# Kernel tuning notes

Measured on AMD Instinct MI355X. Metric: run time of the kernel, lower is better.

## Reference

```python
import jax, jax.numpy as jnp
import numpy as np

H = 132  # hidden size hard-coded in SpatialRelationLayer

def _mlp(x, w1, b1, w2, b2, w3, b3):
    # FCBlock: 2 hidden layers of width 132 with ReLU, then linear out;
    # NNNet wraps it with sigmoid(out * 5)
    h = jax.nn.relu(x @ w1 + b1)
    h = jax.nn.relu(h @ w2 + b2)
    return jax.nn.sigmoid((h @ w3 + b3) * 5.0)

def _mlp_params(key, din, dout):
    k1, k2, k3 = jax.random.split(key, 3)
    def lin(k, i, o):
        kw, kb = jax.random.split(k)
        s = 1.0 / np.sqrt(i)
        return (jax.random.uniform(kw, (i, o), jnp.float32, -s, s),
                jax.random.uniform(kb, (o,), jnp.float32, -s, s))
    w1, b1 = lin(k1, din, H)
    w2, b2 = lin(k2, H, H)
    w3, b3 = lin(k3, H, dout)
    return w1, b1, w2, b2, w3, b3

def setup_inputs() -> dict:
    key = jax.random.key(0)
    b, N, D0, D1, D2 = 8, 128, 128, 128, 64
    O0, O1, O2 = 64, 64, 64
    kP, kQ, kR, kp, kq, kr = jax.random.split(key, 6)
    inp = {
        "P": jax.random.normal(kP, (b, D0), jnp.float32),
        "Q": jax.random.normal(kQ, (b, N, D1), jnp.float32),
        "R": jax.random.normal(kR, (b, N, N, D2), jnp.float32),
    }
    for name, k, din, dout in (("p", kp, D0 + D1, O0),
                               ("q", kq, D1 + D0 + 2 * D2, O1),
                               ("r", kr, D2 + 2 * D1, O2)):
        w1, b1, w2, b2, w3, b3 = _mlp_params(k, din, dout)
        inp.update({f"{name}_w1": w1, f"{name}_b1": b1,
                    f"{name}_w2": w2, f"{name}_b2": b2,
                    f"{name}_w3": w3, f"{name}_b3": b3})
    return inp

def reference(P, Q, R,
              p_w1, p_b1, p_w2, p_b2, p_w3, p_b3,
              q_w1, q_b1, q_w2, q_b2, q_w3, q_b3,
              r_w1, r_b1, r_w2, r_b2, r_w3, r_b3):
    b, N, D1 = Q.shape
    # P branch: global max over objects, concat with P
    P_inputs = jnp.concatenate([jnp.max(Q, axis=1), P], axis=1)  # [b, D1+D0]
    P_out = _mlp(P_inputs, p_w1, p_b1, p_w2, p_b2, p_w3, p_b3)
    # Q branch: broadcast P per-object, max-reduce relations over each axis
    P_exp = jnp.broadcast_to(P[:, None, :], (b, N, P.shape[1]))  # [b,N,D0]
    R_red0 = jnp.max(R, axis=1)  # [b,N,D2]
    R_red1 = jnp.max(R, axis=2)  # [b,N,D2]
    Q_inputs = jnp.concatenate([P_exp, Q, R_red0, R_red1], axis=2)
    Q_out = _mlp(Q_inputs, q_w1, q_b1, q_w2, q_b2, q_w3, q_b3)
    # R branch: pairwise broadcast of Q along both axes, concat with R
    Q0 = jnp.broadcast_to(Q[:, None, :, :], (b, N, N, D1))  # repeat along dim 1
    Q1 = jnp.broadcast_to(Q[:, :, None, :], (b, N, N, D1))  # repeat along dim 2
    R_inputs = jnp.concatenate([R, Q0, Q1], axis=-1)  # [b,N,N,D2+2*D1]
    R_out = _mlp(R_inputs, r_w1, r_b1, r_w2, r_b2, r_w3, r_b3)
    return (P_out, Q_out, R_out)
```

## Files before the change

kernel.cpp:

```cpp
#include <hip/hip_runtime.h>

typedef _Float16 f16;
typedef f16 f16x8 __attribute__((ext_vector_type(8)));
typedef f16 f16x4 __attribute__((ext_vector_type(4)));
typedef float f32x4 __attribute__((ext_vector_type(4)));

#define MFMA16(a, b, c) __builtin_amdgcn_mfma_f32_16x16x32_f16(a, b, c, 0, 0, 0)

#define OFF_RW1A 0
#define OFF_RW2  10240
#define OFF_RW3  35840
#define OFF_QW1  46080
#define OFF_QW2  87040
#define OFF_QW3  112640
#define OFF_PW1  122880
#define OFF_PW2  163840
#define OFF_PW3  189440
#define PACK_BYTES 399360

#define PREP_BLOCKS 2419

struct InPtrs { const float* p[21]; };

__device__ const int g_mSrc[9] = {15, 17, 19, 9, 11, 13, 3, 5, 7};
__device__ const int g_mK0[9]  = {0, 0, 0, 128, 0, 0, 0, 0, 0};
__device__ const int g_mK[9]   = {64, 132, 132, 256, 132, 132, 256, 132, 132};
__device__ const int g_mN[9]   = {132, 132, 64, 132, 132, 64, 132, 132, 64};
__device__ const int g_mNT[9]  = {10, 10, 4, 10, 10, 4, 10, 10, 4};
__device__ const int g_mDst[9] = {OFF_RW1A, OFF_RW2, OFF_RW3, OFF_QW1, OFF_QW2, OFF_QW3,
                                  OFF_PW1, OFF_PW2, OFF_PW3};
__device__ const int g_mBlk0[9] = {1024, 1029, 1042, 1047, 1067, 1080, 1085, 1105, 1118};

__global__ __launch_bounds__(256) void prep_kernel(InPtrs in, f16* __restrict__ wpk,
    float* __restrict__ c1, float* __restrict__ d1, float* __restrict__ e1q,
    float* __restrict__ qmax, float* __restrict__ red0, float* __restrict__ red1)
{
  __shared__ float sbuf[1024];
  const int mb = blockIdx.x, t = threadIdx.x;

  if (mb < 1024) {
    const int b = mb >> 7, j = mb & 127;
    const float* base = in.p[2] + (size_t)b * 128 * 8192 + (size_t)j * 64 + (t & 15) * 4;
    const int g = t >> 4;
    f32x4 mm[8];
    #pragma unroll
    for (int v = 0; v < 8; ++v)
      mm[v] = *(const f32x4*)(base + (size_t)(g + 16 * v) * 8192);
    #pragma unroll
    for (int s = 4; s > 0; s >>= 1)
      #pragma unroll
      for (int v = 0; v < 4; ++v)
        if (v < s) {
          mm[v][0] = fmaxf(mm[v][0], mm[v + s][0]);
          mm[v][1] = fmaxf(mm[v][1], mm[v + s][1]);
          mm[v][2] = fmaxf(mm[v][2], mm[v + s][2]);
          mm[v][3] = fmaxf(mm[v][3], mm[v + s][3]);
        }
    float* sr = sbuf + g * 64 + (t & 15) * 4;
    sr[0] = mm[0][0]; sr[1] = mm[0][1]; sr[2] = mm[0][2]; sr[3] = mm[0][3];
    __syncthreads();
    if (t < 64) {
      float m = sbuf[t];
      #pragma unroll
      for (int g2 = 1; g2 < 16; ++g2) m = fmaxf(m, sbuf[g2 * 64 + t]);
      red0[(size_t)mb * 64 + t] = m;
    }
  } else if (mb < 1123) {
    int mi = 8;
    while (mi > 0 && mb < g_mBlk0[mi]) --mi;
    const int NT = g_mNT[mi], K = g_mK[mi], N = g_mN[mi], K0 = g_mK0[mi];
    const int L = (mb - g_mBlk0[mi]) * 256 + t;
    const int lanes = ((K + 31) >> 5) * NT * 64;
    if (L < lanes) {
      const int lane = L & 63, tile = L >> 6;
      const int kk = tile / NT, nn = tile % NT;
      const float* src = in.p[g_mSrc[mi]];
      const int n = nn * 16 + (lane & 15);
      const int kb = kk * 32 + ((lane >> 4) << 3);
      f16x8 v;
      #pragma unroll
      for (int u = 0; u < 8; ++u) {
        const int k = kb + u;
        float f = (k < K && n < N) ? src[(size_t)(K0 + k) * N + n] : 0.f;
        v[u] = (f16)f;
      }
      *(f16x8*)(wpk + g_mDst[mi] + (size_t)L * 8) = v;
    }
  } else if (mb < 1131) {
    const int b = mb - 1123;
    const float* Qb = in.p[1] + (size_t)b * 128 * 128;
    const int d = t & 127, g = t >> 7;
    float m0 = -3.4e38f, m1 = m0, m2 = m0, m3 = m0;
    #pragma unroll
    for (int v = 0; v < 16; ++v) {
      const int i = g * 64 + v * 4;
      m0 = fmaxf(m0, Qb[(size_t)(i + 0) * 128 + d]);
      m1 = fmaxf(m1, Qb[(size_t)(i + 1) * 128 + d]);
      m2 = fmaxf(m2, Qb[(size_t)(i + 2) * 128 + d]);
      m3 = fmaxf(m3, Qb[(size_t)(i + 3) * 128 + d]);
    }
    sbuf[g * 128 + d] = fmaxf(fmaxf(m0, m1), fmaxf(m2, m3));
    __syncthreads();
    if (t < 128) qmax[b * 128 + t] = fmaxf(sbuf[t], sbuf[128 + t]);
  } else if (mb < 1139) {
    const int b = mb - 1131;
    const float* P = in.p[0]; const float* qw1 = in.p[9]; const float* qb1 = in.p[10];
    if (t < 160) {
      float a = 0.f;
      if (t < 132) {
        float a0 = 0.f, a1 = 0.f, a2 = 0.f, a3 = 0.f;
        for (int k = 0; k < 128; k += 4) {
          a0 += P[b * 128 + k + 0] * qw1[(size_t)(k + 0) * 132 + t];
          a1 += P[b * 128 + k + 1] * qw1[(size_t)(k + 1) * 132 + t];
          a2 += P[b * 128 + k + 2] * qw1[(size_t)(k + 2) * 132 + t];
          a3 += P[b * 128 + k + 3] * qw1[(size_t)(k + 3) * 132 + t];
        }
        a = qb1[t] + (a0 + a1) + (a2 + a3);
      }
      e1q[b * 160 + t] = a;
    }
  } else if (mb < 1395) {
    const int blk = mb - 1139;
    const float* Q = in.p[1]; const float* rw1 = in.p[15]; const float* rb1 = in.p[16];
    for (int o = t; o < 512; o += 256) sbuf[o] = Q[(size_t)blk * 512 + o];
    __syncthreads();
    if (t < 160) {
      float cc[4], dd[4];
      #pragma unroll
      for (int r = 0; r < 4; ++r) { cc[r] = 0.f; dd[r] = 0.f; }
      if (t < 132) {
        const float bb = rb1[t];
        #pragma unroll
        for (int r = 0; r < 4; ++r) cc[r] = bb;
        for (int k = 0; k < 128; ++k) {
          const float wc = rw1[(size_t)(192 + k) * 132 + t];
          const float wd = rw1[(size_t)(64 + k) * 132 + t];
          #pragma unroll
          for (int r = 0; r < 4; ++r) {
            cc[r] += sbuf[r * 128 + k] * wc;
            dd[r] += sbuf[r * 128 + k] * wd;
          }
        }
      }
      for (int r = 0; r < 4; ++r) {
        c1[(size_t)(blk * 4 + r) * 160 + t] = cc[r];
        d1[(size_t)(blk * 4 + r) * 160 + t] = dd[r];
      }
    }
  } else {
    const int blk = mb - 1395;
    const float* base = in.p[2] + (size_t)blk * 8192 + (t & 15) * 4;
    const int g = t >> 4;
    f32x4 mm[8];
    #pragma unroll
    for (int v = 0; v < 8; ++v)
      mm[v] = *(const f32x4*)(base + (size_t)(g + 16 * v) * 64);
    #pragma unroll
    for (int s = 4; s > 0; s >>= 1)
      #pragma unroll
      for (int v = 0; v < 4; ++v)
        if (v < s) {
          mm[v][0] = fmaxf(mm[v][0], mm[v + s][0]);
          mm[v][1] = fmaxf(mm[v][1], mm[v + s][1]);
          mm[v][2] = fmaxf(mm[v][2], mm[v + s][2]);
          mm[v][3] = fmaxf(mm[v][3], mm[v + s][3]);
        }
    float* sr = sbuf + g * 64 + (t & 15) * 4;
    sr[0] = mm[0][0]; sr[1] = mm[0][1]; sr[2] = mm[0][2]; sr[3] = mm[0][3];
    __syncthreads();
    if (t < 64) {
      float m = sbuf[t];
      #pragma unroll
      for (int g2 = 1; g2 < 16; ++g2) m = fmaxf(m, sbuf[g2 * 64 + t]);
      red1[(size_t)blk * 64 + t] = m;
    }
  }
}

__global__ __launch_bounds__(256, 2) void mainR_kernel(const float* __restrict__ R,
    const float* __restrict__ c1, const float* __restrict__ d1,
    const float* __restrict__ rb2, const float* __restrict__ rb3,
    const f16* __restrict__ wpk, float* __restrict__ outR)
{
  __shared__ f16 Xr[128][72];
  __shared__ f16 Hs[128][168];
  const int blk = blockIdx.x;
  const int t = threadIdx.x, lane = t & 63, w = t >> 6;
  const int wm = w >> 1, wn = w & 1;
  const int rbase = wm * 64, nbase = wn * 80;
  const int lr = (lane >> 4) << 2;
  const int lc = lane & 15;
  const int lk = (lane >> 4) << 3;

  const float* Rb = R + (size_t)blk * 8192;
  #pragma unroll
  for (int v = 0; v < 8; ++v) {
    const int quad = v * 256 + t;
    const int j = quad >> 4, kq = quad & 15;
    f32x4 rv = *(const f32x4*)(Rb + (size_t)j * 64 + kq * 4);
    f16x4 hv;
    hv[0] = (f16)rv[0]; hv[1] = (f16)rv[1]; hv[2] = (f16)rv[2]; hv[3] = (f16)rv[3];
    *(f16x4*)(&Xr[j][kq * 4]) = hv;
  }

  const int b = blk >> 7;
  const float* c1r = c1 + (size_t)blk * 160;
  const float* d1b = d1 + (size_t)b * 128 * 160;
  f32x4 acc[4][5];
  #pragma unroll
  for (int mi2 = 0; mi2 < 4; ++mi2) {
    #pragma unroll
    for (int n5 = 0; n5 < 5; ++n5) {
      const int n = nbase + n5 * 16 + lc;
      const float cv = c1r[n];
      #pragma unroll
      for (int r = 0; r < 4; ++r) {
        const int j = rbase + mi2 * 16 + lr + r;
        acc[mi2][n5][r] = cv + d1b[(size_t)j * 160 + n];
      }
    }
  }
  __syncthreads();
  const f16x8* W1p = (const f16x8*)(wpk + OFF_RW1A);
  #pragma unroll
  for (int kk = 0; kk < 2; ++kk) {
    f16x8 a[4];
    #pragma unroll
    for (int mi2 = 0; mi2 < 4; ++mi2)
      a[mi2] = *(const f16x8*)(&Xr[rbase + mi2 * 16 + lc][kk * 32 + lk]);
    #pragma unroll
    for (int n5 = 0; n5 < 5; ++n5) {
      const f16x8 bf = W1p[(size_t)(kk * 10 + wn * 5 + n5) * 64 + lane];
      #pragma unroll
      for (int mi2 = 0; mi2 < 4; ++mi2)
        acc[mi2][n5] = MFMA16(a[mi2], bf, acc[mi2][n5]);
    }
  }
  #pragma unroll
  for (int mi2 = 0; mi2 < 4; ++mi2)
    #pragma unroll
    for (int n5 = 0; n5 < 5; ++n5)
      #pragma unroll
      for (int r = 0; r < 4; ++r)
        Hs[rbase + mi2 * 16 + lr + r][nbase + n5 * 16 + lc] =
            (f16)fmaxf(acc[mi2][n5][r], 0.f);
  __syncthreads();

  #pragma unroll
  for (int mi2 = 0; mi2 < 4; ++mi2)
    #pragma unroll
    for (int n5 = 0; n5 < 5; ++n5) {
      const int n = nbase + n5 * 16 + lc;
      const float bv = (n < 132) ? rb2[n] : 0.f;
      #pragma unroll
      for (int r = 0; r < 4; ++r) acc[mi2][n5][r] = bv;
    }
  const f16x8* W2p = (const f16x8*)(wpk + OFF_RW2);
  #pragma unroll
  for (int kk = 0; kk < 5; ++kk) {
    f16x8 a[4];
    #pragma unroll
    for (int mi2 = 0; mi2 < 4; ++mi2)
      a[mi2] = *(const f16x8*)(&Hs[rbase + mi2 * 16 + lc][kk * 32 + lk]);
    #pragma unroll
    for (int n5 = 0; n5 < 5; ++n5) {
      const f16x8 bf = W2p[(size_t)(kk * 10 + wn * 5 + n5) * 64 + lane];
      #pragma unroll
      for (int mi2 = 0; mi2 < 4; ++mi2)
        acc[mi2][n5] = MFMA16(a[mi2], bf, acc[mi2][n5]);
    }
  }
  __syncthreads();
  #pragma unroll
  for (int mi2 = 0; mi2 < 4; ++mi2)
    #pragma unroll
    for (int n5 = 0; n5 < 5; ++n5)
      #pragma unroll
      for (int r = 0; r < 4; ++r)
        Hs[rbase + mi2 * 16 + lr + r][nbase + n5 * 16 + lc] =
            (f16)fmaxf(acc[mi2][n5][r], 0.f);
  __syncthreads();

  f32x4 acc3[4][2];
  const int n3base = wn * 32;
  #pragma unroll
  for (int mi2 = 0; mi2 < 4; ++mi2)
    #pragma unroll
    for (int n2 = 0; n2 < 2; ++n2) {
      const float bv = rb3[n3base + n2 * 16 + lc];
      #pragma unroll
      for (int r = 0; r < 4; ++r) acc3[mi2][n2][r] = bv;
    }
  const f16x8* W3p = (const f16x8*)(wpk + OFF_RW3);
  #pragma unroll
  for (int kk = 0; kk < 5; ++kk) {
    f16x8 a[4];
    #pragma unroll
    for (int mi2 = 0; mi2 < 4; ++mi2)
      a[mi2] = *(const f16x8*)(&Hs[rbase + mi2 * 16 + lc][kk * 32 + lk]);
    #pragma unroll
    for (int n2 = 0; n2 < 2; ++n2) {
      const f16x8 bf = W3p[(size_t)(kk * 4 + wn * 2 + n2) * 64 + lane];
      #pragma unroll
      for (int mi2 = 0; mi2 < 4; ++mi2)
        acc3[mi2][n2] = MFMA16(a[mi2], bf, acc3[mi2][n2]);
    }
  }
  float* Ro = outR + (size_t)blk * 8192;
  #pragma unroll
  for (int mi2 = 0; mi2 < 4; ++mi2)
    #pragma unroll
    for (int n2 = 0; n2 < 2; ++n2)
      #pragma unroll
      for (int r = 0; r < 4; ++r) {
        const int j = rbase + mi2 * 16 + lr + r;
        const int n = n3base + n2 * 16 + lc;
        Ro[(size_t)j * 64 + n] = 1.f / (1.f + __expf(-5.f * acc3[mi2][n2][r]));
      }
}

__global__ __launch_bounds__(256) void small_kernel(const float* __restrict__ P,
    const float* __restrict__ Q,
    const float* __restrict__ qb2, const float* __restrict__ qb3,
    const float* __restrict__ pb1, const float* __restrict__ pb2, const float* __restrict__ pb3,
    const f16* __restrict__ wpk, const float* __restrict__ e1q, const float* __restrict__ qmax,
    const float* __restrict__ red0, const float* __restrict__ red1,
    float* __restrict__ outP, float* __restrict__ outQ)
{
  __shared__ f16 Xc[64][72];
  __shared__ f16 Hs2[64][168];
  __shared__ f16 Wb[40960];
  const int blk = blockIdx.x;
  const bool isP = (blk == 16);
  const int t = threadIdx.x, lane = t & 63, w = t >> 6;
  const int wm = w >> 1, wn = w & 1;
  const int rb = wm * 32;
  const int lr = (lane >> 4) << 2, lc = lane & 15, lk = (lane >> 4) << 3;
  const int b = blk >> 1, x0 = (blk & 1) * 64;
  const f16* W1g = wpk + (isP ? OFF_PW1 : OFF_QW1);
  const f16* W2g = wpk + (isP ? OFF_PW2 : OFF_QW2);
  const f16* W3g = wpk + (isP ? OFF_PW3 : OFF_QW3);

  for (int f = w; f < 80; f += 4)
    *(f16x8*)(&Wb[f * 512 + lane * 8]) = *(const f16x8*)(W1g + (size_t)f * 512 + lane * 8);

  f32x4 acc[2][5];
  #pragma unroll
  for (int mi2 = 0; mi2 < 2; ++mi2)
    #pragma unroll
    for (int n5 = 0; n5 < 5; ++n5) {
      const int n = (wn * 5 + n5) * 16 + lc;
      const float cv = isP ? ((n < 132) ? pb1[n] : 0.f) : e1q[b * 160 + n];
      #pragma unroll
      for (int r = 0; r < 4; ++r) acc[mi2][n5][r] = cv;
    }

  for (int c = 0; c < 4; ++c) {
    __syncthreads();
    for (int o = t; o < 1024; o += 256) {
      const int rr = o >> 4, kq = o & 15;
      f32x4 v = {0.f, 0.f, 0.f, 0.f};
      if (isP) {
        if (rr < 8) {
          const float* s = (c < 2) ? (qmax + rr * 128 + c * 64) : (P + rr * 128 + (c - 2) * 64);
          v = *(const f32x4*)(s + kq * 4);
        }
      } else {
        const size_t rowg = (size_t)(b * 128 + x0 + rr);
        const float* s = (c < 2) ? (Q + rowg * 128 + c * 64)
                                 : (((c == 2) ? red0 : red1) + rowg * 64);
        v = *(const f32x4*)(s + kq * 4);
      }
      f16x4 hv;
      hv[0] = (f16)v[0]; hv[1] = (f16)v[1]; hv[2] = (f16)v[2]; hv[3] = (f16)v[3];
      *(f16x4*)(&Xc[rr][kq * 4]) = hv;
    }
    __syncthreads();
    #pragma unroll
    for (int kk = 0; kk < 2; ++kk) {
      f16x8 a[2];
      #pragma unroll
      for (int mi2 = 0; mi2 < 2; ++mi2)
        a[mi2] = *(const f16x8*)(&Xc[rb + mi2 * 16 + lc][kk * 32 + lk]);
      const int kg = c * 2 + kk;
      #pragma unroll
      for (int n5 = 0; n5 < 5; ++n5) {
        const f16x8 bf = *(const f16x8*)(&Wb[(kg * 10 + wn * 5 + n5) * 512 + lane * 8]);
        #pragma unroll
        for (int mi2 = 0; mi2 < 2; ++mi2)
          acc[mi2][n5] = MFMA16(a[mi2], bf, acc[mi2][n5]);
      }
    }
  }
  #pragma unroll
  for (int mi2 = 0; mi2 < 2; ++mi2)
    #pragma unroll
    for (int n5 = 0; n5 < 5; ++n5)
      #pragma unroll
      for (int r = 0; r < 4; ++r)
        Hs2[rb + mi2 * 16 + lr + r][(wn * 5 + n5) * 16 + lc] = (f16)fmaxf(acc[mi2][n5][r], 0.f);
  __syncthreads();

  for (int f = w; f < 50; f += 4)
    *(f16x8*)(&Wb[f * 512 + lane * 8]) = *(const f16x8*)(W2g + (size_t)f * 512 + lane * 8);
  for (int f = w; f < 20; f += 4)
    *(f16x8*)(&Wb[(50 + f) * 512 + lane * 8]) = *(const f16x8*)(W3g + (size_t)f * 512 + lane * 8);

  #pragma unroll
  for (int mi2 = 0; mi2 < 2; ++mi2)
    #pragma unroll
    for (int n5 = 0; n5 < 5; ++n5) {
      const int n = (wn * 5 + n5) * 16 + lc;
      const float bv = (n < 132) ? (isP ? pb2[n] : qb2[n]) : 0.f;
      #pragma unroll
      for (int r = 0; r < 4; ++r) acc[mi2][n5][r] = bv;
    }
  __syncthreads();
  #pragma unroll
  for (int kk = 0; kk < 5; ++kk) {
    f16x8 a[2];
    #pragma unroll
    for (int mi2 = 0; mi2 < 2; ++mi2)
      a[mi2] = *(const f16x8*)(&Hs2[rb + mi2 * 16 + lc][kk * 32 + lk]);
    #pragma unroll
    for (int n5 = 0; n5 < 5; ++n5) {
      const f16x8 bf = *(const f16x8*)(&Wb[(kk * 10 + wn * 5 + n5) * 512 + lane * 8]);
      #pragma unroll
      for (int mi2 = 0; mi2 < 2; ++mi2)
        acc[mi2][n5] = MFMA16(a[mi2], bf, acc[mi2][n5]);
    }
  }
  __syncthreads();
  #pragma unroll
  for (int mi2 = 0; mi2 < 2; ++mi2)
    #pragma unroll
    for (int n5 = 0; n5 < 5; ++n5)
      #pragma unroll
      for (int r = 0; r < 4; ++r)
        Hs2[rb + mi2 * 16 + lr + r][(wn * 5 + n5) * 16 + lc] = (f16)fmaxf(acc[mi2][n5][r], 0.f);
  __syncthreads();

  f32x4 acc3[2][2];
  #pragma unroll
  for (int mi2 = 0; mi2 < 2; ++mi2)
    #pragma unroll
    for (int j2 = 0; j2 < 2; ++j2) {
      const int n = (wn * 2 + j2) * 16 + lc;
      const float bv = isP ? pb3[n] : qb3[n];
      #pragma unroll
      for (int r = 0; r < 4; ++r) acc3[mi2][j2][r] = bv;
    }
  #pragma unroll
  for (int kk = 0; kk < 5; ++kk) {
    f16x8 a[2];
    #pragma unroll
    for (int mi2 = 0; mi2 < 2; ++mi2)
      a[mi2] = *(const f16x8*)(&Hs2[rb + mi2 * 16 + lc][kk * 32 + lk]);
    #pragma unroll
    for (int j2 = 0; j2 < 2; ++j2) {
      const f16x8 bf = *(const f16x8*)(&Wb[(50 + kk * 4 + wn * 2 + j2) * 512 + lane * 8]);
      #pragma unroll
      for (int mi2 = 0; mi2 < 2; ++mi2)
        acc3[mi2][j2] = MFMA16(a[mi2], bf, acc3[mi2][j2]);
    }
  }
  #pragma unroll
  for (int mi2 = 0; mi2 < 2; ++mi2)
    #pragma unroll
    for (int j2 = 0; j2 < 2; ++j2)
      #pragma unroll
      for (int r = 0; r < 4; ++r) {
        const int rr = rb + mi2 * 16 + lr + r;
        const int n = (wn * 2 + j2) * 16 + lc;
        const float s = 1.f / (1.f + __expf(-5.f * acc3[mi2][j2][r]));
        if (isP) {
          if (rr < 8) outP[rr * 64 + n] = s;
        } else {
          outQ[((size_t)(b * 128 + x0 + rr)) * 64 + n] = s;
        }
      }
}

extern "C" void kernel_launch(void* const* d_in, const int* in_sizes, int n_in,
                              void* d_out, int out_size, void* d_ws, size_t ws_size,
                              hipStream_t stream) {
  (void)in_sizes; (void)n_in; (void)out_size; (void)ws_size;
  InPtrs ip;
  for (int i = 0; i < 21; ++i) ip.p[i] = (const float*)d_in[i];

  char* ws = (char*)d_ws;
  f16* wpk = (f16*)ws;
  float* wsf = (float*)(ws + PACK_BYTES);
  float* c1 = wsf;
  float* d1 = wsf + 163840;
  float* e1q = wsf + 327680;
  float* qmax = wsf + 328960;
  float* red0 = wsf + 329984;
  float* red1 = wsf + 395520;

  float* outP = (float*)d_out;
  float* outQ = outP + 512;
  float* outR = outP + 66048;

  prep_kernel<<<dim3(PREP_BLOCKS), dim3(256), 0, stream>>>(ip, wpk, c1, d1, e1q, qmax, red0, red1);
  mainR_kernel<<<dim3(1024), dim3(256), 0, stream>>>((const float*)d_in[2], c1, d1,
      (const float*)d_in[18], (const float*)d_in[20], wpk, outR);
  small_kernel<<<dim3(17), dim3(256), 0, stream>>>((const float*)d_in[0], (const float*)d_in[1],
      (const float*)d_in[12], (const float*)d_in[14],
      (const float*)d_in[4], (const float*)d_in[6], (const float*)d_in[8],
      wpk, e1q, qmax, red0, red1, outP, outQ);
}
```

Before: 73.63 us.

## Merge R and Q/P MLP kernels into one launch with transposed MFMA operands

Combines the R-branch kernel and the small Q/P-branch kernel into a single launch of 1041 blocks that branch on block index and share one 80KB LDS pool. This removes a kernel launch and the tail gap between the two kernels. The MFMA operands are also swapped so each lane holds four consecutive output columns, which allows vectorized f32x4 bias and d1 loads, f16x4 LDS stores and f32x4 global output stores. The small-branch W1 staging is cut to half-size chunks to fit the shared pool. The larger static LDS allocation may lower occupancy for the R blocks.

```diff
diff --git a/kernel.cpp b/kernel.cpp
--- a/kernel.cpp
+++ b/kernel.cpp
@@ -177,308 +177,322 @@
   }
 }
 
-__global__ __launch_bounds__(256, 2) void mainR_kernel(const float* __restrict__ R,
-    const float* __restrict__ c1, const float* __restrict__ d1,
+__device__ __forceinline__ float sig5(float x) {
+  return 1.f / (1.f + __expf(-5.f * x));
+}
+
+__global__ __launch_bounds__(256, 2) void fused_kernel(
+    const float* __restrict__ R, const float* __restrict__ c1, const float* __restrict__ d1,
     const float* __restrict__ rb2, const float* __restrict__ rb3,
-    const f16* __restrict__ wpk, float* __restrict__ outR)
+    const f16* __restrict__ wpk, float* __restrict__ outR,
+    const float* __restrict__ P, const float* __restrict__ Q,
+    const float* __restrict__ qb2, const float* __restrict__ qb3,
+    const float* __restrict__ pb1, const float* __restrict__ pb2, const float* __restrict__ pb3,
+    const float* __restrict__ e1q, const float* __restrict__ qmax,
+    const float* __restrict__ red0, const float* __restrict__ red1,
+    float* __restrict__ outP, float* __restrict__ outQ)
 {
-  __shared__ f16 Xr[128][72];
-  __shared__ f16 Hs[128][168];
+  __shared__ __align__(16) char pool[81920];
   const int blk = blockIdx.x;
   const int t = threadIdx.x, lane = t & 63, w = t >> 6;
   const int wm = w >> 1, wn = w & 1;
-  const int rbase = wm * 64, nbase = wn * 80;
   const int lr = (lane >> 4) << 2;
   const int lc = lane & 15;
   const int lk = (lane >> 4) << 3;
 
-  const float* Rb = R + (size_t)blk * 8192;
-  #pragma unroll
-  for (int v = 0; v < 8; ++v) {
-    const int quad = v * 256 + t;
-    const int j = quad >> 4, kq = quad & 15;
-    f32x4 rv = *(const f32x4*)(Rb + (size_t)j * 64 + kq * 4);
-    f16x4 hv;
-    hv[0] = (f16)rv[0]; hv[1] = (f16)rv[1]; hv[2] = (f16)rv[2]; hv[3] = (f16)rv[3];
-    *(f16x4*)(&Xr[j][kq * 4]) = hv;
+  if (blk < 1024) {
+    f16 (*Xr)[72]  = (f16(*)[72])pool;
+    f16 (*Hs)[168] = (f16(*)[168])(pool + 18432);
+    const int rbase = wm * 64, nbase = wn * 80;
+
+    const float* Rb = R + (size_t)blk * 8192;
+    #pragma unroll
+    for (int v = 0; v < 8; ++v) {
+      const int quad = v * 256 + t;
+      const int j = quad >> 4, kq = quad & 15;
+      f32x4 rv = *(const f32x4*)(Rb + (size_t)j * 64 + kq * 4);
+      f16x4 hv;
+      hv[0] = (f16)rv[0]; hv[1] = (f16)rv[1]; hv[2] = (f16)rv[2]; hv[3] = (f16)rv[3];
+      *(f16x4*)(&Xr[j][kq * 4]) = hv;
+    }
+
+    const int b = blk >> 7;
+    const float* c1r = c1 + (size_t)blk * 160;
+    const float* d1b = d1 + (size_t)b * 128 * 160;
+    f32x4 acc[4][5];
+    f32x4 cvv[5];
+    #pragma unroll
+    for (int n5 = 0; n5 < 5; ++n5)
+      cvv[n5] = *(const f32x4*)(c1r + nbase + n5 * 16 + lr);
+    #pragma unroll
+    for (int mi2 = 0; mi2 < 4; ++mi2) {
+      const int j = rbase + mi2 * 16 + lc;
+      #pragma unroll
+      for (int n5 = 0; n5 < 5; ++n5) {
+        f32x4 dv = *(const f32x4*)(d1b + (size_t)j * 160 + nbase + n5 * 16 + lr);
+        acc[mi2][n5] = cvv[n5] + dv;
+      }
+    }
+    __syncthreads();
+    const f16x8* W1p = (const f16x8*)(wpk + OFF_RW1A);
+    #pragma unroll
+    for (int kk = 0; kk < 2; ++kk) {
+      f16x8 a[4];
+      #pragma unroll
+      for (int mi2 = 0; mi2 < 4; ++mi2)
+        a[mi2] = *(const f16x8*)(&Xr[rbase + mi2 * 16 + lc][kk * 32 + lk]);
+      #pragma unroll
+      for (int n5 = 0; n5 < 5; ++n5) {
+        const f16x8 bf = W1p[(size_t)(kk * 10 + wn * 5 + n5) * 64 + lane];
+        #pragma unroll
+        for (int mi2 = 0; mi2 < 4; ++mi2)
+          acc[mi2][n5] = MFMA16(bf, a[mi2], acc[mi2][n5]);
+      }
+    }
+    #pragma unroll
+    for (int mi2 = 0; mi2 < 4; ++mi2) {
+      const int j = rbase + mi2 * 16 + lc;
+      #pragma unroll
+      for (int n5 = 0; n5 < 5; ++n5) {
+        f16x4 hv;
+        #pragma unroll
+        for (int r = 0; r < 4; ++r) hv[r] = (f16)fmaxf(acc[mi2][n5][r], 0.f);
+        *(f16x4*)(&Hs[j][nbase + n5 * 16 + lr]) = hv;
+      }
+    }
+    __syncthreads();
+
+    #pragma unroll
+    for (int n5 = 0; n5 < 5; ++n5) {
+      const int nb = nbase + n5 * 16 + lr;
+      f32x4 bv = {0.f, 0.f, 0.f, 0.f};
+      if (nb < 132) bv = *(const f32x4*)(rb2 + nb);
+      #pragma unroll
+      for (int mi2 = 0; mi2 < 4; ++mi2) acc[mi2][n5] = bv;
+    }
+    const f16x8* W2p = (const f16x8*)(wpk + OFF_RW2);
+    #pragma unroll
+    for (int kk = 0; kk < 5; ++kk) {
+      f16x8 a[4];
+      #pragma unroll
+      for (int mi2 = 0; mi2 < 4; ++mi2)
+        a[mi2] = *(const f16x8*)(&Hs[rbase + mi2 * 16 + lc][kk * 32 + lk]);
+      #pragma unroll
+      for (int n5 = 0; n5 < 5; ++n5) {
+        const f16x8 bf = W2p[(size_t)(kk * 10 + wn * 5 + n5) * 64 + lane];
+        #pragma unroll
+        for (int mi2 = 0; mi2 < 4; ++mi2)
+          acc[mi2][n5] = MFMA16(bf, a[mi2], acc[mi2][n5]);
+      }
+    }
+    __syncthreads();
+    #pragma unroll
+    for (int mi2 = 0; mi2 < 4; ++mi2) {
+      const int j = rbase + mi2 * 16 + lc;
+      #pragma unroll
+      for (int n5 = 0; n5 < 5; ++n5) {
+        f16x4 hv;
+        #pragma unroll
+        for (int r = 0; r < 4; ++r) hv[r] = (f16)fmaxf(acc[mi2][n5][r], 0.f);
+        *(f16x4*)(&Hs[j][nbase + n5 * 16 + lr]) = hv;
+      }
+    }
+    __syncthreads();
+
+    f32x4 acc3[4][2];
+    const int n3base = wn * 32;
+    #pragma unroll
+    for (int n2 = 0; n2 < 2; ++n2) {
+      f32x4 bv = *(const f32x4*)(rb3 + n3base + n2 * 16 + lr);
+      #pragma unroll
+      for (int mi2 = 0; mi2 < 4; ++mi2) acc3[mi2][n2] = bv;
+    }
+    const f16x8* W3p = (const f16x8*)(wpk + OFF_RW3);
+    #pragma unroll
+    for (int kk = 0; kk < 5; ++kk) {
+      f16x8 a[4];
+      #pragma unroll
+      for (int mi2 = 0; mi2 < 4; ++mi2)
+        a[mi2] = *(const f16x8*)(&Hs[rbase + mi2 * 16 + lc][kk * 32 + lk]);
+      #pragma unroll
+      for (int n2 = 0; n2 < 2; ++n2) {
+        const f16x8 bf = W3p[(size_t)(kk * 4 + wn * 2 + n2) * 64 + lane];
+        #pragma unroll
+        for (int mi2 = 0; mi2 < 4; ++mi2)
+          acc3[mi2][n2] = MFMA16(bf, a[mi2], acc3[mi2][n2]);
+      }
+    }
+    float* Ro = outR + (size_t)blk * 8192;
+    #pragma unroll
+    for (int mi2 = 0; mi2 < 4; ++mi2) {
+      const int j = rbase + mi2 * 16 + lc;
+      #pragma unroll
+      for (int n2 = 0; n2 < 2; ++n2) {
+        f32x4 ov;
+        #pragma unroll
+        for (int r = 0; r < 4; ++r) ov[r] = sig5(acc3[mi2][n2][r]);
+        *(f32x4*)(Ro + (size_t)j * 64 + n3base + n2 * 16 + lr) = ov;
+      }
+    }
+  } else {
+    f16 (*Xc)[72]  = (f16(*)[72])pool;
+    f16 (*Hs2)[168] = (f16(*)[168])(pool + 9216);
+    f16* Wb = (f16*)(pool + 30720);
+    const int bs = blk - 1024;
+    const bool isP = (bs == 16);
+    const int rb = wm * 32;
+    const int b = bs >> 1, x0 = (bs & 1) * 64;
+    const f16* W1g = wpk + (isP ? OFF_PW1 : OFF_QW1);
+    const f16* W2g = wpk + (isP ? OFF_PW2 : OFF_QW2);
+    const f16* W3g = wpk + (isP ? OFF_PW3 : OFF_QW3);
+
+    f32x4 acc[2][5];
+    #pragma unroll
+    for (int n5 = 0; n5 < 5; ++n5) {
+      const int nb = wn * 80 + n5 * 16 + lr;
+      f32x4 cv = {0.f, 0.f, 0.f, 0.f};
+      if (isP) { if (nb < 132) cv = *(const f32x4*)(pb1 + nb); }
+      else cv = *(const f32x4*)(e1q + b * 160 + nb);
+      acc[0][n5] = cv; acc[1][n5] = cv;
+    }
+
+    for (int c = 0; c < 4; ++c) {
+      if ((c & 1) == 0) {
+        const int half = c >> 1;
+        for (int idx = t; idx < 40 * 64; idx += 256) {
+          const int f = idx >> 6, ln = idx & 63;
+          *(f16x8*)(&Wb[f * 512 + ln * 8]) =
+              *(const f16x8*)(W1g + (size_t)(half * 40 + f) * 512 + ln * 8);
+        }
+      }
+      for (int o = t; o < 1024; o += 256) {
+        const int rr = o >> 4, kq = o & 15;
+        f32x4 v = {0.f, 0.f, 0.f, 0.f};
+        if (isP) {
+          if (rr < 8) {
+            const float* s = (c < 2) ? (qmax + rr * 128 + c * 64) : (P + rr * 128 + (c - 2) * 64);
+            v = *(const f32x4*)(s + kq * 4);
+          }
+        } else {
+          const size_t rowg = (size_t)(b * 128 + x0 + rr);
+          const float* s = (c < 2) ? (Q + rowg * 128 + c * 64)
+                                   : (((c == 2) ? red0 : red1) + rowg * 64);
+          v = *(const f32x4*)(s + kq * 4);
+        }
+        f16x4 hv;
+        hv[0] = (f16)v[0]; hv[1] = (f16)v[1]; hv[2] = (f16)v[2]; hv[3] = (f16)v[3];
+        *(f16x4*)(&Xc[rr][kq * 4]) = hv;
+      }
+      __syncthreads();
+      #pragma unroll
+      for (int kk = 0; kk < 2; ++kk) {
+        f16x8 a[2];
+        #pragma unroll
+        for (int mi2 = 0; mi2 < 2; ++mi2)
+          a[mi2] = *(const f16x8*)(&Xc[rb + mi2 * 16 + lc][kk * 32 + lk]);
+        #pragma unroll
+        for (int n5 = 0; n5 < 5; ++n5) {
+          const int rel = ((c & 1) * 2 + kk) * 10 + wn * 5 + n5;
+          const f16x8 bf = *(const f16x8*)(&Wb[rel * 512 + lane * 8]);
+          #pragma unroll
+          for (int mi2 = 0; mi2 < 2; ++mi2)
+            acc[mi2][n5] = MFMA16(bf, a[mi2], acc[mi2][n5]);
+        }
+      }
+      __syncthreads();
+    }
+    #pragma unroll
+    for (int mi2 = 0; mi2 < 2; ++mi2) {
+      const int j = rb + mi2 * 16 + lc;
+      #pragma unroll
+      for (int n5 = 0; n5 < 5; ++n5) {
+        f16x4 hv;
+        #pragma unroll
+        for (int r = 0; r < 4; ++r) hv[r] = (f16)fmaxf(acc[mi2][n5][r], 0.f);
+        *(f16x4*)(&Hs2[j][wn * 80 + n5 * 16 + lr]) = hv;
+      }
+    }
+    for (int idx = t; idx < 50 * 64; idx += 256) {
+      const int f = idx >> 6, ln = idx & 63;
+      *(f16x8*)(&Wb[f * 512 + ln * 8]) = *(const f16x8*)(W2g + (size_t)f * 512 + ln * 8);
+    }
+    #pragma unroll
+    for (int n5 = 0; n5 < 5; ++n5) {
+      const int nb = wn * 80 + n5 * 16 + lr;
+      f32x4 bv = {0.f, 0.f, 0.f, 0.f};
+      if (nb < 132) bv = *(const f32x4*)((isP ? pb2 : qb2) + nb);
+      acc[0][n5] = bv; acc[1][n5] = bv;
+    }
+    __syncthreads();
+    #pragma unroll
+    for (int kk = 0; kk < 5; ++kk) {
+      f16x8 a[2];
+      #pragma unroll
+      for (int mi2 = 0; mi2 < 2; ++mi2)
+        a[mi2] = *(const f16x8*)(&Hs2[rb + mi2 * 16 + lc][kk * 32 + lk]);
+      #pragma unroll
+      for (int n5 = 0; n5 < 5; ++n5) {
+        const f16x8 bf = *(const f16x8*)(&Wb[(kk * 10 + wn * 5 + n5) * 512 + lane * 8]);
+        #pragma unroll
+        for (int mi2 = 0; mi2 < 2; ++mi2)
+          acc[mi2][n5] = MFMA16(bf, a[mi2], acc[mi2][n5]);
+      }
+    }
+    __syncthreads();
+    #pragma unroll
+    for (int mi2 = 0; mi2 < 2; ++mi2) {
+      const int j = rb + mi2 * 16 + lc;
+      #pragma unroll
+      for (int n5 = 0; n5 < 5; ++n5) {
+        f16x4 hv;
+        #pragma unroll
+        for (int r = 0; r < 4; ++r) hv[r] = (f16)fmaxf(acc[mi2][n5][r], 0.f);
+        *(f16x4*)(&Hs2[j][wn * 80 + n5 * 16 + lr]) = hv;
+      }
+    }
+    for (int idx = t; idx < 20 * 64; idx += 256) {
+      const int f = idx >> 6, ln = idx & 63;
+      *(f16x8*)(&Wb[f * 512 + ln * 8]) = *(const f16x8*)(W3g + (size_t)f * 512 + ln * 8);
+    }
+    __syncthreads();
+
+    f32x4 acc3[2][2];
+    const int n3base = wn * 32;
+    #pragma unroll
+    for (int n2 = 0; n2 < 2; ++n2) {
+      f32x4 bv = *(const f32x4*)((isP ? pb3 : qb3) + n3base + n2 * 16 + lr);
+      acc3[0][n2] = bv; acc3[1][n2] = bv;
+    }
+    #pragma unroll
+    for (int kk = 0; kk < 5; ++kk) {
+      f16x8 a[2];
+      #pragma unroll
+      for (int mi2 = 0; mi2 < 2; ++mi2)
+        a[mi2] = *(const f16x8*)(&Hs2[rb + mi2 * 16 + lc][kk * 32 + lk]);
+      #pragma unroll
+      for (int n2 = 0; n2 < 2; ++n2) {
+        const f16x8 bf = *(const f16x8*)(&Wb[(kk * 4 + wn * 2 + n2) * 512 + lane * 8]);
+        #pragma unroll
+        for (int mi2 = 0; mi2 < 2; ++mi2)
+          acc3[mi2][n2] = MFMA16(bf, a[mi2], acc3[mi2][n2]);
+      }
+    }
+    #pragma unroll
+    for (int mi2 = 0; mi2 < 2; ++mi2) {
+      const int j = rb + mi2 * 16 + lc;
+      #pragma unroll
+      for (int n2 = 0; n2 < 2; ++n2) {
+        f32x4 ov;
+        #pragma unroll
+        for (int r = 0; r < 4; ++r) ov[r] = sig5(acc3[mi2][n2][r]);
+        if (isP) {
+          if (j < 8) *(f32x4*)(outP + (size_t)j * 64 + n3base + n2 * 16 + lr) = ov;
+        } else {
+          *(f32x4*)(outQ + ((size_t)(b * 128 + x0 + j)) * 64 + n3base + n2 * 16 + lr) = ov;
+        }
+      }
+    }
   }
-
-  const int b = blk >> 7;
-  const float* c1r = c1 + (size_t)blk * 160;
-  const float* d1b = d1 + (size_t)b * 128 * 160;
-  f32x4 acc[4][5];
-  #pragma unroll
-  for (int mi2 = 0; mi2 < 4; ++mi2) {
-    #pragma unroll
-    for (int n5 = 0; n5 < 5; ++n5) {
-      const int n = nbase + n5 * 16 + lc;
-      const float cv = c1r[n];
-      #pragma unroll
-      for (int r = 0; r < 4; ++r) {
-        const int j = rbase + mi2 * 16 + lr + r;
-        acc[mi2][n5][r] = cv + d1b[(size_t)j * 160 + n];
-      }
-    }
-  }
-  __syncthreads();
-  const f16x8* W1p = (const f16x8*)(wpk + OFF_RW1A);
-  #pragma unroll
-  for (int kk = 0; kk < 2; ++kk) {
-    f16x8 a[4];
-    #pragma unroll
-    for (int mi2 = 0; mi2 < 4; ++mi2)
-      a[mi2] = *(const f16x8*)(&Xr[rbase + mi2 * 16 + lc][kk * 32 + lk]);
-    #pragma unroll
-    for (int n5 = 0; n5 < 5; ++n5) {
-      const f16x8 bf = W1p[(size_t)(kk * 10 + wn * 5 + n5) * 64 + lane];
-      #pragma unroll
-      for (int mi2 = 0; mi2 < 4; ++mi2)
-        acc[mi2][n5] = MFMA16(a[mi2], bf, acc[mi2][n5]);
-    }
-  }
-  #pragma unroll
-  for (int mi2 = 0; mi2 < 4; ++mi2)
-    #pragma unroll
-    for (int n5 = 0; n5 < 5; ++n5)
-      #pragma unroll
-      for (int r = 0; r < 4; ++r)
-        Hs[rbase + mi2 * 16 + lr + r][nbase + n5 * 16 + lc] =
-            (f16)fmaxf(acc[mi2][n5][r], 0.f);
-  __syncthreads();
-
-  #pragma unroll
-  for (int mi2 = 0; mi2 < 4; ++mi2)
-    #pragma unroll
-    for (int n5 = 0; n5 < 5; ++n5) {
-      const int n = nbase + n5 * 16 + lc;
-      const float bv = (n < 132) ? rb2[n] : 0.f;
-      #pragma unroll
-      for (int r = 0; r < 4; ++r) acc[mi2][n5][r] = bv;
-    }
-  const f16x8* W2p = (const f16x8*)(wpk + OFF_RW2);
-  #pragma unroll
-  for (int kk = 0; kk < 5; ++kk) {
-    f16x8 a[4];
-    #pragma unroll
-    for (int mi2 = 0; mi2 < 4; ++mi2)
-      a[mi2] = *(const f16x8*)(&Hs[rbase + mi2 * 16 + lc][kk * 32 + lk]);
-    #pragma unroll
-    for (int n5 = 0; n5 < 5; ++n5) {
-      const f16x8 bf = W2p[(size_t)(kk * 10 + wn * 5 + n5) * 64 + lane];
-      #pragma unroll
-      for (int mi2 = 0; mi2 < 4; ++mi2)
-        acc[mi2][n5] = MFMA16(a[mi2], bf, acc[mi2][n5]);
-    }
-  }
-  __syncthreads();
-  #pragma unroll
-  for (int mi2 = 0; mi2 < 4; ++mi2)
-    #pragma unroll
-    for (int n5 = 0; n5 < 5; ++n5)
-      #pragma unroll
-      for (int r = 0; r < 4; ++r)
-        Hs[rbase + mi2 * 16 + lr + r][nbase + n5 * 16 + lc] =
-            (f16)fmaxf(acc[mi2][n5][r], 0.f);
-  __syncthreads();
-
-  f32x4 acc3[4][2];
-  const int n3base = wn * 32;
-  #pragma unroll
-  for (int mi2 = 0; mi2 < 4; ++mi2)
-    #pragma unroll
-    for (int n2 = 0; n2 < 2; ++n2) {
-      const float bv = rb3[n3base + n2 * 16 + lc];
-      #pragma unroll
-      for (int r = 0; r < 4; ++r) acc3[mi2][n2][r] = bv;
-    }
-  const f16x8* W3p = (const f16x8*)(wpk + OFF_RW3);
-  #pragma unroll
-  for (int kk = 0; kk < 5; ++kk) {
-    f16x8 a[4];
-    #pragma unroll
-    for (int mi2 = 0; mi2 < 4; ++mi2)
-      a[mi2] = *(const f16x8*)(&Hs[rbase + mi2 * 16 + lc][kk * 32 + lk]);
-    #pragma unroll
-    for (int n2 = 0; n2 < 2; ++n2) {
-      const f16x8 bf = W3p[(size_t)(kk * 4 + wn * 2 + n2) * 64 + lane];
-      #pragma unroll
-      for (int mi2 = 0; mi2 < 4; ++mi2)
-        acc3[mi2][n2] = MFMA16(a[mi2], bf, acc3[mi2][n2]);
-    }
-  }
-  float* Ro = outR + (size_t)blk * 8192;
-  #pragma unroll
-  for (int mi2 = 0; mi2 < 4; ++mi2)
-    #pragma unroll
-    for (int n2 = 0; n2 < 2; ++n2)
-      #pragma unroll
-      for (int r = 0; r < 4; ++r) {
-        const int j = rbase + mi2 * 16 + lr + r;
-        const int n = n3base + n2 * 16 + lc;
-        Ro[(size_t)j * 64 + n] = 1.f / (1.f + __expf(-5.f * acc3[mi2][n2][r]));
-      }
-}
-
-__global__ __launch_bounds__(256) void small_kernel(const float* __restrict__ P,
-    const float* __restrict__ Q,
-    const float* __restrict__ qb2, const float* __restrict__ qb3,
-    const float* __restrict__ pb1, const float* __restrict__ pb2, const float* __restrict__ pb3,
-    const f16* __restrict__ wpk, const float* __restrict__ e1q, const float* __restrict__ qmax,
-    const float* __restrict__ red0, const float* __restrict__ red1,
-    float* __restrict__ outP, float* __restrict__ outQ)
-{
-  __shared__ f16 Xc[64][72];
-  __shared__ f16 Hs2[64][168];
-  __shared__ f16 Wb[40960];
-  const int blk = blockIdx.x;
-  const bool isP = (blk == 16);
-  const int t = threadIdx.x, lane = t & 63, w = t >> 6;
-  const int wm = w >> 1, wn = w & 1;
-  const int rb = wm * 32;
-  const int lr = (lane >> 4) << 2, lc = lane & 15, lk = (lane >> 4) << 3;
-  const int b = blk >> 1, x0 = (blk & 1) * 64;
-  const f16* W1g = wpk + (isP ? OFF_PW1 : OFF_QW1);
-  const f16* W2g = wpk + (isP ? OFF_PW2 : OFF_QW2);
-  const f16* W3g = wpk + (isP ? OFF_PW3 : OFF_QW3);
-
-  for (int f = w; f < 80; f += 4)
-    *(f16x8*)(&Wb[f * 512 + lane * 8]) = *(const f16x8*)(W1g + (size_t)f * 512 + lane * 8);
-
-  f32x4 acc[2][5];
-  #pragma unroll
-  for (int mi2 = 0; mi2 < 2; ++mi2)
-    #pragma unroll
-    for (int n5 = 0; n5 < 5; ++n5) {
-      const int n = (wn * 5 + n5) * 16 + lc;
-      const float cv = isP ? ((n < 132) ? pb1[n] : 0.f) : e1q[b * 160 + n];
-      #pragma unroll
-      for (int r = 0; r < 4; ++r) acc[mi2][n5][r] = cv;
-    }
-
-  for (int c = 0; c < 4; ++c) {
-    __syncthreads();
-    for (int o = t; o < 1024; o += 256) {
-      const int rr = o >> 4, kq = o & 15;
-      f32x4 v = {0.f, 0.f, 0.f, 0.f};
-      if (isP) {
-        if (rr < 8) {
-          const float* s = (c < 2) ? (qmax + rr * 128 + c * 64) : (P + rr * 128 + (c - 2) * 64);
-          v = *(const f32x4*)(s + kq * 4);
-        }
-      } else {
-        const size_t rowg = (size_t)(b * 128 + x0 + rr);
-        const float* s = (c < 2) ? (Q + rowg * 128 + c * 64)
-                                 : (((c == 2) ? red0 : red1) + rowg * 64);
-        v = *(const f32x4*)(s + kq * 4);
-      }
-      f16x4 hv;
-      hv[0] = (f16)v[0]; hv[1] = (f16)v[1]; hv[2] = (f16)v[2]; hv[3] = (f16)v[3];
-      *(f16x4*)(&Xc[rr][kq * 4]) = hv;
-    }
-    __syncthreads();
-    #pragma unroll
-    for (int kk = 0; kk < 2; ++kk) {
-      f16x8 a[2];
-      #pragma unroll
-      for (int mi2 = 0; mi2 < 2; ++mi2)
-        a[mi2] = *(const f16x8*)(&Xc[rb + mi2 * 16 + lc][kk * 32 + lk]);
-      const int kg = c * 2 + kk;
-      #pragma unroll
-      for (int n5 = 0; n5 < 5; ++n5) {
-        const f16x8 bf = *(const f16x8*)(&Wb[(kg * 10 + wn * 5 + n5) * 512 + lane * 8]);
-        #pragma unroll
-        for (int mi2 = 0; mi2 < 2; ++mi2)
-          acc[mi2][n5] = MFMA16(a[mi2], bf, acc[mi2][n5]);
-      }
-    }
-  }
-  #pragma unroll
-  for (int mi2 = 0; mi2 < 2; ++mi2)
-    #pragma unroll
-    for (int n5 = 0; n5 < 5; ++n5)
-      #pragma unroll
-      for (int r = 0; r < 4; ++r)
-        Hs2[rb + mi2 * 16 + lr + r][(wn * 5 + n5) * 16 + lc] = (f16)fmaxf(acc[mi2][n5][r], 0.f);
-  __syncthreads();
-
-  for (int f = w; f < 50; f += 4)
-    *(f16x8*)(&Wb[f * 512 + lane * 8]) = *(const f16x8*)(W2g + (size_t)f * 512 + lane * 8);
-  for (int f = w; f < 20; f += 4)
-    *(f16x8*)(&Wb[(50 + f) * 512 + lane * 8]) = *(const f16x8*)(W3g + (size_t)f * 512 + lane * 8);
-
-  #pragma unroll
-  for (int mi2 = 0; mi2 < 2; ++mi2)
-    #pragma unroll
-    for (int n5 = 0; n5 < 5; ++n5) {
-      const int n = (wn * 5 + n5) * 16 + lc;
-      const float bv = (n < 132) ? (isP ? pb2[n] : qb2[n]) : 0.f;
-      #pragma unroll
-      for (int r = 0; r < 4; ++r) acc[mi2][n5][r] = bv;
-    }
-  __syncthreads();
-  #pragma unroll
-  for (int kk = 0; kk < 5; ++kk) {
-    f16x8 a[2];
-    #pragma unroll
-    for (int mi2 = 0; mi2 < 2; ++mi2)
-      a[mi2] = *(const f16x8*)(&Hs2[rb + mi2 * 16 + lc][kk * 32 + lk]);
-    #pragma unroll
-    for (int n5 = 0; n5 < 5; ++n5) {
-      const f16x8 bf = *(const f16x8*)(&Wb[(kk * 10 + wn * 5 + n5) * 512 + lane * 8]);
-      #pragma unroll
-      for (int mi2 = 0; mi2 < 2; ++mi2)
-        acc[mi2][n5] = MFMA16(a[mi2], bf, acc[mi2][n5]);
-    }
-  }
-  __syncthreads();
-  #pragma unroll
-  for (int mi2 = 0; mi2 < 2; ++mi2)
-    #pragma unroll
-    for (int n5 = 0; n5 < 5; ++n5)
-      #pragma unroll
-      for (int r = 0; r < 4; ++r)
-        Hs2[rb + mi2 * 16 + lr + r][(wn * 5 + n5) * 16 + lc] = (f16)fmaxf(acc[mi2][n5][r], 0.f);
-  __syncthreads();
-
-  f32x4 acc3[2][2];
-  #pragma unroll
-  for (int mi2 = 0; mi2 < 2; ++mi2)
-    #pragma unroll
-    for (int j2 = 0; j2 < 2; ++j2) {
-      const int n = (wn * 2 + j2) * 16 + lc;
-      const float bv = isP ? pb3[n] : qb3[n];
-      #pragma unroll
-      for (int r = 0; r < 4; ++r) acc3[mi2][j2][r] = bv;
-    }
-  #pragma unroll
-  for (int kk = 0; kk < 5; ++kk) {
-    f16x8 a[2];
-    #pragma unroll
-    for (int mi2 = 0; mi2 < 2; ++mi2)
-      a[mi2] = *(const f16x8*)(&Hs2[rb + mi2 * 16 + lc][kk * 32 + lk]);
-    #pragma unroll
-    for (int j2 = 0; j2 < 2; ++j2) {
-      const f16x8 bf = *(const f16x8*)(&Wb[(50 + kk * 4 + wn * 2 + j2) * 512 + lane * 8]);
-      #pragma unroll
-      for (int mi2 = 0; mi2 < 2; ++mi2)
-        acc3[mi2][j2] = MFMA16(a[mi2], bf, acc3[mi2][j2]);
-    }
-  }
-  #pragma unroll
-  for (int mi2 = 0; mi2 < 2; ++mi2)
-    #pragma unroll
-    for (int j2 = 0; j2 < 2; ++j2)
-      #pragma unroll
-      for (int r = 0; r < 4; ++r) {
-        const int rr = rb + mi2 * 16 + lr + r;
-        const int n = (wn * 2 + j2) * 16 + lc;
-        const float s = 1.f / (1.f + __expf(-5.f * acc3[mi2][j2][r]));
-        if (isP) {
-          if (rr < 8) outP[rr * 64 + n] = s;
-        } else {
-          outQ[((size_t)(b * 128 + x0 + rr)) * 64 + n] = s;
-        }
-      }
 }
 
 extern "C" void kernel_launch(void* const* d_in, const int* in_sizes, int n_in,
@@ -503,10 +517,10 @@
   float* outR = outP + 66048;
 
   prep_kernel<<<dim3(PREP_BLOCKS), dim3(256), 0, stream>>>(ip, wpk, c1, d1, e1q, qmax, red0, red1);
-  mainR_kernel<<<dim3(1024), dim3(256), 0, stream>>>((const float*)d_in[2], c1, d1,
-      (const float*)d_in[18], (const float*)d_in[20], wpk, outR);
-  small_kernel<<<dim3(17), dim3(256), 0, stream>>>((const float*)d_in[0], (const float*)d_in[1],
+  fused_kernel<<<dim3(1041), dim3(256), 0, stream>>>((const float*)d_in[2], c1, d1,
+      (const float*)d_in[18], (const float*)d_in[20], wpk, outR,
+      (const float*)d_in[0], (const float*)d_in[1],
       (const float*)d_in[12], (const float*)d_in[14],
       (const float*)d_in[4], (const float*)d_in[6], (const float*)d_in[8],
-      wpk, e1q, qmax, red0, red1, outP, outQ);
+      e1q, qmax, red0, red1, outP, outQ);
 }
```

After: 73.55 us. About the same (-0.1%).
